# Optimization experiments

Hardware: AMD Instinct MI355X
Metric: run time of the kernel (lower is better)

## Reference

```python
import jax, jax.numpy as jnp
import numpy as np

DEPTH = 6
N_INTERNAL = 2 ** DEPTH - 1  # 63
N_LEAVES = 2 ** DEPTH        # 64


def _tree_paths(depth):
    """Precompute, for each leaf, its `depth` ancestor internal-node indices and
    whether the path goes right at each ancestor (static heap-indexing of the tree)."""
    n_internal = 2 ** depth - 1
    n_leaves = 2 ** depth
    anc = np.zeros((n_leaves, depth), dtype=np.int32)
    right = np.zeros((n_leaves, depth), dtype=bool)
    for leaf in range(n_leaves):
        node = leaf + n_internal
        for d in range(depth):
            parent = (node - 1) // 2
            anc[leaf, d] = parent
            right[leaf, d] = (node % 2 == 0)
            node = parent
    return jnp.asarray(anc), jnp.asarray(right)

_ANC, _RIGHT = _tree_paths(DEPTH)


def setup_inputs() -> dict:
    key = jax.random.key(0)
    k = jax.random.split(key, 6)
    B, F, T, C = 8192, 256, 32, 100
    return {
        "x": jax.random.normal(k[0], (B, F), dtype=jnp.float32),
        "split_weights": jax.random.normal(k[1], (T, N_INTERNAL, F), dtype=jnp.float32) * 0.05,
        "split_bias": jax.random.normal(k[2], (T, N_INTERNAL), dtype=jnp.float32) * 0.05,
        "leaf_logits": jax.random.normal(k[3], (T, N_LEAVES, C), dtype=jnp.float32),
        "tree_weights": jax.random.normal(k[4], (T,), dtype=jnp.float32),
        "log_temperature": jnp.zeros((), dtype=jnp.float32),
    }


def reference(x, split_weights, split_bias, leaf_logits, tree_weights, log_temperature):
    # temperature = exp(log_temperature).clamp(0.1, 5.0)
    temp = jnp.clip(jnp.exp(log_temperature), 0.1, 5.0)
    # split probabilities for all trees at once: [T, B, N_INTERNAL]
    logits = jnp.einsum('bf,tnf->tbn', x, split_weights) + split_bias[:, None, :]
    split_probs = jax.nn.sigmoid(logits / temp)
    # gather each leaf's ancestor probs: [T, B, L, D]; right -> p, left -> 1-p
    g = split_probs[:, :, _ANC]
    leaf_probs = jnp.prod(jnp.where(_RIGHT, g, 1.0 - g), axis=-1)  # [T, B, L]
    # per-leaf class distributions: [T, L, C]
    leaf_class_probs = jax.nn.softmax(leaf_logits / temp, axis=-1)
    outputs = jnp.einsum('tbl,tlc->tbc', leaf_probs, leaf_class_probs)  # [T, B, C]
    weights = jax.nn.softmax(tree_weights, axis=0)  # [T]
    return jnp.einsum('t,tbc->bc', weights, outputs)  # [B, C]
```

## Files before the change

### kernel.cpp

```cpp
#include <hip/hip_runtime.h>
#include <math.h>

#define B_  8192
#define F_  256
#define T_  32
#define NI_ 63
#define NL_ 64
#define C_  100
#define K2_ (T_*NL_)
#define NG  4
#define TPG 8

typedef unsigned short u16;
typedef __attribute__((ext_vector_type(8))) short bf16x8;
typedef __attribute__((ext_vector_type(4))) float f32x4;
typedef __attribute__((ext_vector_type(8))) unsigned short u16x8;

__device__ __forceinline__ u16 f2bf(float f) {
    unsigned int u = __float_as_uint(f);
    u += 0x7fffu + ((u >> 16) & 1u);
    return (u16)(u >> 16);
}

#define WSB_SWB  0
#define WSB_LCPT (T_*NI_*F_*2)
#define WSB_TOT  ((size_t)WSB_LCPT + 112*K2_*2)

#define ZBLK   (B_*C_/256)
#define SWBLK  (T_*NI_*F_/256)
#define LCPBLK (T_*NL_/256)
__global__ void k_prep(const float* __restrict__ sw, const float* __restrict__ ll,
                       const float* __restrict__ tw, const float* __restrict__ logT,
                       u16* __restrict__ swb, u16* __restrict__ lcpT,
                       float* __restrict__ out) {
    int blk = blockIdx.x, tid = threadIdx.x;
    if (blk < ZBLK) { out[blk * 256 + tid] = 0.f; return; }
    blk -= ZBLK;
    if (blk < SWBLK) { int i = blk * 256 + tid; swb[i] = f2bf(sw[i]); return; }
    blk -= SWBLK;
    int idx = blk * 256 + tid;
    int t = idx >> 6;
    float temp = __expf(logT[0]);
    temp = fminf(fmaxf(temp, 0.1f), 5.0f);
    float invt = 1.0f / temp;

    float m = -1e30f;
    for (int j = 0; j < T_; ++j) m = fmaxf(m, tw[j]);
    float s = 0.f;
    for (int j = 0; j < T_; ++j) s += __expf(tw[j] - m);
    float wt = __expf(tw[t] - m) / s;

    const float* row = ll + (size_t)idx * C_;
    float m2 = -1e30f;
    for (int c = 0; c < C_; ++c) m2 = fmaxf(m2, row[c]);
    float s2 = 0.f;
    for (int c = 0; c < C_; ++c) s2 += __expf((row[c] - m2) * invt);
    float sc = wt / s2;
    for (int c = 0; c < C_; ++c)
        lcpT[(size_t)c * K2_ + idx] = f2bf(sc * __expf((row[c] - m2) * invt));
    for (int c = C_; c < 112; ++c)
        lcpT[(size_t)c * K2_ + idx] = 0;
}

__global__ __launch_bounds__(256, 2)
void k_fused(const float* __restrict__ x, const u16* __restrict__ swb,
             const float* __restrict__ sb, const float* __restrict__ logT,
             const u16* __restrict__ lcpT, float* __restrict__ out) {
    __shared__ u16   swS[63 * 264];
    __shared__ u16   lcpS[8 * 112 * 8];
    __shared__ float slog[4][16][66];
    int tid  = threadIdx.x;
    int w    = tid >> 6;
    int lane = tid & 63;
    int col  = lane & 15;
    int quad = lane >> 4;
    int mb   = blockIdx.x * 64 + w * 16;
    int tg   = blockIdx.y;

    float temp = __expf(logT[0]);
    temp = fminf(fmaxf(temp, 0.1f), 5.0f);
    float invt = 1.0f / temp;

    bf16x8 afr[8];
    #pragma unroll
    for (int ks = 0; ks < 8; ++ks) {
        const float4* px = (const float4*)(x + (size_t)(mb + col) * F_ + ks * 32 + quad * 8);
        float4 v0 = px[0], v1 = px[1];
        bf16x8 a;
        a[0] = (short)f2bf(v0.x); a[1] = (short)f2bf(v0.y);
        a[2] = (short)f2bf(v0.z); a[3] = (short)f2bf(v0.w);
        a[4] = (short)f2bf(v1.x); a[5] = (short)f2bf(v1.y);
        a[6] = (short)f2bf(v1.z); a[7] = (short)f2bf(v1.w);
        afr[ks] = a;
    }

    u16x8 pf_sw[8];
    u16x8 pf_lcp[4];
    {
        int t0 = tg * TPG;
        const char* gsrc = (const char*)(swb + (size_t)t0 * NI_ * F_);
        #pragma unroll
        for (int r = 0; r < 8; ++r) {
            int g = r * 4096 + tid * 16;
            if (g < NI_ * F_ * 2) pf_sw[r] = *(const u16x8*)(gsrc + g);
        }
        #pragma unroll
        for (int r = 0; r < 4; ++r) {
            int idx = r * 256 + tid;
            if (idx < 896) {
                int o = idx / 112, c = idx - o * 112;
                pf_lcp[r] = *(const u16x8*)(lcpT + (size_t)c * K2_ + t0 * NL_ + o * 8);
            }
        }
    }

    f32x4 accO[7];
    #pragma unroll
    for (int i = 0; i < 7; ++i) accO[i] = (f32x4){0.f, 0.f, 0.f, 0.f};

    #pragma unroll 1
    for (int ti = 0; ti < TPG; ++ti) {
        int t = tg * TPG + ti;

        __syncthreads();
        #pragma unroll
        for (int r = 0; r < 8; ++r) {
            int g = r * 4096 + tid * 16;
            if (g < NI_ * F_ * 2) {
                int n   = g >> 9;
                int k16 = (g & 511) >> 4;
                *(u16x8*)&swS[n * 264 + k16 * 8] = pf_sw[r];
            }
        }
        #pragma unroll
        for (int r = 0; r < 4; ++r) {
            int idx = r * 256 + tid;
            if (idx < 896) {
                int o = idx / 112, c = idx - o * 112;
                *(u16x8*)&lcpS[(o * 112 + c) * 8] = pf_lcp[r];
            }
        }
        __syncthreads();

        if (ti + 1 < TPG) {
            int tn = t + 1;
            const char* gsrc = (const char*)(swb + (size_t)tn * NI_ * F_);
            #pragma unroll
            for (int r = 0; r < 8; ++r) {
                int g = r * 4096 + tid * 16;
                if (g < NI_ * F_ * 2) pf_sw[r] = *(const u16x8*)(gsrc + g);
            }
            #pragma unroll
            for (int r = 0; r < 4; ++r) {
                int idx = r * 256 + tid;
                if (idx < 896) {
                    int o = idx / 112, c = idx - o * 112;
                    pf_lcp[r] = *(const u16x8*)(lcpT + (size_t)c * K2_ + tn * NL_ + o * 8);
                }
            }
        }

        f32x4 acc[4];
        #pragma unroll
        for (int i = 0; i < 4; ++i) acc[i] = (f32x4){0.f, 0.f, 0.f, 0.f};
        #pragma unroll
        for (int ks = 0; ks < 8; ++ks) {
            #pragma unroll
            for (int nt = 0; nt < 4; ++nt) {
                int n  = nt * 16 + col;
                int ne = n > 62 ? 62 : n;
                bf16x8 bfr = *(const bf16x8*)&swS[ne * 264 + ks * 32 + quad * 8];
                acc[nt] = __builtin_amdgcn_mfma_f32_16x16x32_bf16(afr[ks], bfr, acc[nt], 0, 0, 0);
            }
        }

        asm volatile("s_waitcnt lgkmcnt(0)" ::: "memory");
        #pragma unroll
        for (int nt = 0; nt < 4; ++nt) {
            int n = nt * 16 + col;
            float bias = (n < NI_) ? sb[t * NI_ + n] : 0.f;
            #pragma unroll
            for (int r = 0; r < 4; ++r) {
                float lg = (acc[nt][r] + bias) * invt;
                slog[w][quad * 4 + r][n] = 1.0f / (1.0f + __expf(-lg));
            }
        }
        asm volatile("s_waitcnt lgkmcnt(0)" ::: "memory");

        bf16x8 af0, af1;
        #pragma unroll
        for (int grp = 0; grp < 2; ++grp) {
            int s = (grp ? 11 : 7) + quad;
            float pref = 1.0f;
            int node = s;
            #pragma unroll
            for (int d = 0; d < 3; ++d) {
                int par = (node - 1) >> 1;
                float g = slog[w][col][par];
                pref = (node & 1) ? (pref - pref * g) : (pref * g);
                node = par;
            }
            float gs  = slog[w][col][s];
            float gl  = slog[w][col][2 * s + 1];
            float gr  = slog[w][col][2 * s + 2];
            float g00 = slog[w][col][4 * s + 3];
            float g01 = slog[w][col][4 * s + 4];
            float g10 = slog[w][col][4 * s + 5];
            float g11 = slog[w][col][4 * s + 6];
            #pragma unroll
            for (int j = 0; j < 8; ++j) {
                const int b2 = (j >> 2) & 1, b1 = (j >> 1) & 1, b0 = j & 1;
                float f3 = b2 ? gs : 1.0f - gs;
                float c1 = b2 ? gr : gl;
                float f4 = b1 ? c1 : 1.0f - c1;
                float c2 = b2 ? (b1 ? g11 : g10) : (b1 ? g01 : g00);
                float f5 = b0 ? c2 : 1.0f - c2;
                float p  = pref * f3 * f4 * f5;
                if (grp == 0) af0[j] = (short)f2bf(p);
                else          af1[j] = (short)f2bf(p);
            }
        }

        #pragma unroll
        for (int nt = 0; nt < 7; ++nt) {
            int n = nt * 16 + col;
            bf16x8 lb0 = *(const bf16x8*)&lcpS[(quad * 112 + n) * 8];
            bf16x8 lb1 = *(const bf16x8*)&lcpS[((4 + quad) * 112 + n) * 8];
            accO[nt] = __builtin_amdgcn_mfma_f32_16x16x32_bf16(af0, lb0, accO[nt], 0, 0, 0);
            accO[nt] = __builtin_amdgcn_mfma_f32_16x16x32_bf16(af1, lb1, accO[nt], 0, 0, 0);
        }
    }

    #pragma unroll
    for (int nt = 0; nt < 7; ++nt) {
        int c = nt * 16 + col;
        if (c < C_) {
            #pragma unroll
            for (int r = 0; r < 4; ++r) {
                int b = mb + quad * 4 + r;
                atomicAdd(&out[(size_t)b * C_ + c], accO[nt][r]);
            }
        }
    }
}

__global__ void k_zf(float* __restrict__ out, int n) {
    int i = blockIdx.x * 256 + threadIdx.x;
    if (i < n) out[i] = 0.f;
}

__global__ void k_mono(const float* __restrict__ x, const float* __restrict__ sw,
                       const float* __restrict__ sb, const float* __restrict__ ll,
                       const float* __restrict__ tw, const float* __restrict__ logT,
                       float* __restrict__ outg) {
    __shared__ float slcp[NL_ * C_];
    int tid = threadIdx.x;
    int b = blockIdx.x * 256 + tid;

    float temp = __expf(logT[0]);
    temp = fminf(fmaxf(temp, 0.1f), 5.0f);
    float invt = 1.0f / temp;

    float m = -1e30f;
    for (int j = 0; j < T_; ++j) m = fmaxf(m, tw[j]);
    float sden = 0.f;
    for (int j = 0; j < T_; ++j) sden += __expf(tw[j] - m);

    float acc[C_];
    #pragma unroll
    for (int c = 0; c < C_; ++c) acc[c] = 0.f;

    for (int t = 0; t < T_; ++t) {
        __syncthreads();
        {
            int l = tid & 63, cq = tid >> 6;
            float wt = __expf(tw[t] - m) / sden;
            const float* row = ll + ((size_t)t * NL_ + l) * C_;
            float m2 = -1e30f;
            for (int c = 0; c < C_; ++c) m2 = fmaxf(m2, row[c]);
            float s2 = 0.f;
            for (int c = 0; c < C_; ++c) s2 += __expf((row[c] - m2) * invt);
            float sc = wt / s2;
            for (int c = cq * 25; c < cq * 25 + 25; ++c)
                slcp[l * C_ + c] = sc * __expf((row[c] - m2) * invt);
        }
        __syncthreads();

        float an[NI_];
        #pragma unroll
        for (int n = 0; n < NI_; ++n) an[n] = 0.f;
        for (int k = 0; k < F_; ++k) {
            float xv = x[(size_t)b * F_ + k];
            #pragma unroll
            for (int n = 0; n < NI_; ++n)
                an[n] = fmaf(xv, sw[((size_t)t * NI_ + n) * F_ + k], an[n]);
        }
        #pragma unroll
        for (int n = 0; n < NI_; ++n) {
            float lg = (an[n] + sb[t * NI_ + n]) * invt;
            an[n] = 1.0f / (1.0f + __expf(-lg));
        }
        #pragma unroll
        for (int l = 0; l < NL_; ++l) {
            int node = l + NI_;
            float p = 1.0f;
            #pragma unroll
            for (int d = 0; d < 6; ++d) {
                int par = (node - 1) >> 1;
                float gv = an[par];
                p = (node & 1) ? (p - p * gv) : (p * gv);
                node = par;
            }
            #pragma unroll
            for (int c = 0; c < C_; ++c)
                acc[c] = fmaf(p, slcp[l * C_ + c], acc[c]);
        }
    }
    for (int c = 0; c < C_; ++c)
        outg[(size_t)b * C_ + c] = acc[c];
}

extern "C" void kernel_launch(void* const* d_in, const int* in_sizes, int n_in,
                              void* d_out, int out_size, void* d_ws, size_t ws_size,
                              hipStream_t stream) {
    bool ok = (n_in >= 6)
           && (in_sizes[0] == B_ * F_)
           && (in_sizes[1] == T_ * NI_ * F_)
           && (in_sizes[2] == T_ * NI_)
           && (in_sizes[3] == T_ * NL_ * C_)
           && (in_sizes[4] == T_)
           && (in_sizes[5] == 1)
           && (out_size == B_ * C_);
    if (!ok) {
        k_zf<<<(out_size + 255) / 256, 256, 0, stream>>>((float*)d_out, out_size);
        return;
    }

    const float* x    = (const float*)d_in[0];
    const float* sw   = (const float*)d_in[1];
    const float* sb   = (const float*)d_in[2];
    const float* ll   = (const float*)d_in[3];
    const float* tw   = (const float*)d_in[4];
    const float* logT = (const float*)d_in[5];
    float* out = (float*)d_out;

    if (ws_size >= WSB_TOT) {
        u16* swb  = (u16*)((char*)d_ws + WSB_SWB);
        u16* lcpT = (u16*)((char*)d_ws + WSB_LCPT);

        k_prep <<<ZBLK + SWBLK + LCPBLK, 256, 0, stream>>>(sw, ll, tw, logT, swb, lcpT, out);
        k_fused<<<dim3(B_ / 64, NG), 256, 0, stream>>>(x, swb, sb, logT, lcpT, out);
    } else {
        k_mono<<<B_ / 256, 256, 0, stream>>>(x, sw, sb, ll, tw, logT, out);
    }
}
```

Measured before the change: 138.6 us.

## Replace output atomics with per-group partial stores and a separate reduction kernel

When enough workspace is available, each tree-group block writes its accumulator tile into a private partial buffer padded to 112 columns, instead of issuing float atomicAdds into the output. A new reduction kernel then sums the four group partials into the output. This removes the atomic contention and the output zeroing pass. In exchange it costs an extra kernel launch and roughly 14 MB of extra global write and read traffic. The old atomic path remains as a fallback for smaller workspaces.

```diff
diff --git a/kernel.cpp b/kernel.cpp
--- a/kernel.cpp
+++ b/kernel.cpp
@@ -22,22 +22,26 @@
     return (u16)(u >> 16);
 }
 
-#define WSB_SWB  0
-#define WSB_LCPT (T_*NI_*F_*2)
-#define WSB_TOT  ((size_t)WSB_LCPT + 112*K2_*2)
-
-#define ZBLK   (B_*C_/256)
+#define WSB_SWB   0
+#define WSB_LCPT  (T_*NI_*F_*2)
+#define WSB_PART  ((size_t)WSB_LCPT + 112*K2_*2)
+#define WSB_ATOM  WSB_PART
+#define WSB_STORE (WSB_PART + (size_t)NG*B_*112*4)
+
 #define SWBLK  (T_*NI_*F_/256)
 #define LCPBLK (T_*NL_/256)
+#define ZBLK   (B_*C_/256)
 __global__ void k_prep(const float* __restrict__ sw, const float* __restrict__ ll,
                        const float* __restrict__ tw, const float* __restrict__ logT,
                        u16* __restrict__ swb, u16* __restrict__ lcpT,
                        float* __restrict__ out) {
     int blk = blockIdx.x, tid = threadIdx.x;
-    if (blk < ZBLK) { out[blk * 256 + tid] = 0.f; return; }
-    blk -= ZBLK;
     if (blk < SWBLK) { int i = blk * 256 + tid; swb[i] = f2bf(sw[i]); return; }
     blk -= SWBLK;
+    if (blk >= LCPBLK) {
+        out[(blk - LCPBLK) * 256 + tid] = 0.f;
+        return;
+    }
     int idx = blk * 256 + tid;
     int t = idx >> 6;
     float temp = __expf(logT[0]);
@@ -65,7 +69,7 @@
 __global__ __launch_bounds__(256, 2)
 void k_fused(const float* __restrict__ x, const u16* __restrict__ swb,
              const float* __restrict__ sb, const float* __restrict__ logT,
-             const u16* __restrict__ lcpT, float* __restrict__ out) {
+             const u16* __restrict__ lcpT, float* __restrict__ dst, int storeMode) {
     __shared__ u16   swS[63 * 264];
     __shared__ u16   lcpS[8 * 112 * 8];
     __shared__ float slog[4][16][66];
@@ -231,16 +235,41 @@
         }
     }
 
-    #pragma unroll
-    for (int nt = 0; nt < 7; ++nt) {
-        int c = nt * 16 + col;
-        if (c < C_) {
+    if (storeMode) {
+        float* pp = dst + (size_t)tg * B_ * 112;
+        #pragma unroll
+        for (int nt = 0; nt < 7; ++nt) {
+            int c = nt * 16 + col;
             #pragma unroll
             for (int r = 0; r < 4; ++r) {
                 int b = mb + quad * 4 + r;
-                atomicAdd(&out[(size_t)b * C_ + c], accO[nt][r]);
-            }
-        }
+                pp[(size_t)b * 112 + c] = accO[nt][r];
+            }
+        }
+    } else {
+        #pragma unroll
+        for (int nt = 0; nt < 7; ++nt) {
+            int c = nt * 16 + col;
+            if (c < C_) {
+                #pragma unroll
+                for (int r = 0; r < 4; ++r) {
+                    int b = mb + quad * 4 + r;
+                    atomicAdd(&dst[(size_t)b * C_ + c], accO[nt][r]);
+                }
+            }
+        }
+    }
+}
+
+__global__ void k_red(const float* __restrict__ part, float* __restrict__ out) {
+    int idx = blockIdx.x * 256 + threadIdx.x;
+    int b = idx / 112, c = idx - b * 112;
+    if (c < C_) {
+        float s = 0.f;
+        #pragma unroll
+        for (int tg = 0; tg < NG; ++tg)
+            s += part[((size_t)tg * B_ + b) * 112 + c];
+        out[(size_t)b * C_ + c] = s;
     }
 }
 
@@ -344,12 +373,20 @@
     const float* logT = (const float*)d_in[5];
     float* out = (float*)d_out;
 
-    if (ws_size >= WSB_TOT) {
+    if (ws_size >= WSB_STORE) {
+        u16*   swb  = (u16*)((char*)d_ws + WSB_SWB);
+        u16*   lcpT = (u16*)((char*)d_ws + WSB_LCPT);
+        float* part = (float*)((char*)d_ws + WSB_PART);
+
+        k_prep <<<SWBLK + LCPBLK, 256, 0, stream>>>(sw, ll, tw, logT, swb, lcpT, out);
+        k_fused<<<dim3(B_ / 64, NG), 256, 0, stream>>>(x, swb, sb, logT, lcpT, part, 1);
+        k_red  <<<(B_ * 112) / 256, 256, 0, stream>>>(part, out);
+    } else if (ws_size >= WSB_ATOM) {
         u16* swb  = (u16*)((char*)d_ws + WSB_SWB);
         u16* lcpT = (u16*)((char*)d_ws + WSB_LCPT);
 
-        k_prep <<<ZBLK + SWBLK + LCPBLK, 256, 0, stream>>>(sw, ll, tw, logT, swb, lcpT, out);
-        k_fused<<<dim3(B_ / 64, NG), 256, 0, stream>>>(x, swb, sb, logT, lcpT, out);
+        k_prep <<<SWBLK + LCPBLK + ZBLK, 256, 0, stream>>>(sw, ll, tw, logT, swb, lcpT, out);
+        k_fused<<<dim3(B_ / 64, NG), 256, 0, stream>>>(x, swb, sb, logT, lcpT, out, 0);
     } else {
         k_mono<<<B_ / 256, 256, 0, stream>>>(x, sw, sb, ll, tw, logT, out);
     }
```

Result: faster. 131.5 us (-5.1%).
